# Kernel tuning notes

Hardware: AMD Instinct MI355X
Metric: run time of the kernel (lower is better)

## Reference

```python
import jax, jax.numpy as jnp
import numpy as np

N_STU, N_ITEM, N_CONC = 10000, 50000, 2048
EDGES, K = 250000, 4
EMB, CNUM = 64, 128


def setup_inputs() -> dict:
    key = jax.random.key(0)
    ks = jax.random.split(key, 10)
    return {
        "stu_idx": jax.random.randint(ks[0], (EDGES,), 0, N_STU),
        "item_idx": jax.random.randint(ks[1], (EDGES,), 0, N_ITEM),
        "conc_idx": jax.random.randint(ks[2], (EDGES, K), 0, N_CONC),
        "stu_fusion": jax.random.normal(ks[3], (N_STU, EMB), jnp.float32),
        "item_fusion": jax.random.normal(ks[4], (N_ITEM, EMB), jnp.float32),
        "concept_fusion": jax.random.normal(ks[5], (N_CONC, EMB), jnp.float32),
        # factor weights are non-negative in the original (NoneNegClipper)
        "W_stu": jax.random.uniform(ks[6], (CNUM, 2 * EMB), jnp.float32) * 0.1,
        "W_item": jax.random.uniform(ks[7], (CNUM, 2 * EMB), jnp.float32) * 0.1,
        "w_pred": jax.random.uniform(ks[8], (CNUM,), jnp.float32) * 0.1,
        "b_pred": jax.random.normal(ks[9], (1,), jnp.float32),
    }


def reference(stu_idx, item_idx, conc_idx, stu_fusion, item_fusion,
              concept_fusion, W_stu, W_item, w_pred, b_pred):
    emb = stu_fusion.shape[1]
    # split Linear(2*emb -> CNUM) into the two cat halves: out = x1 @ Wa.T + x2 @ Wb.T
    Ws_a, Ws_b = W_stu[:, :emb], W_stu[:, emb:]
    Wi_a, Wi_b = W_item[:, :emb], W_item[:, emb:]

    # per-entity projections computed once on the tables, then gathered (cheap)
    stu_part = (stu_fusion @ Ws_a.T)[stu_idx]      # [E, CNUM]
    item_part = (item_fusion @ Wi_a.T)[item_idx]   # [E, CNUM]
    conc_stu = (concept_fusion @ Ws_b.T)[conc_idx]   # [E, K, CNUM]
    conc_item = (concept_fusion @ Wi_b.T)[conc_idx]  # [E, K, CNUM]

    stu_out = jax.nn.sigmoid(stu_part[:, None, :] + conc_stu)    # [E, K, CNUM]
    item_out = jax.nn.sigmoid(item_part[:, None, :] + conc_item)  # [E, K, CNUM]
    diff = stu_out - item_out
    per_conc = jax.nn.sigmoid(jnp.einsum('ekc,c->ek', diff, w_pred) + b_pred[0])  # [E, K]
    return per_conc.mean(axis=1)  # [E]
```

## Files before the change

### kernel.cpp

```cpp
#include <hip/hip_runtime.h>
#include <hip/hip_bf16.h>
#include <hip/hip_fp16.h>

constexpr int EDGES = 250000;
constexpr int EMB   = 64;
constexpr int CNUM  = 128;
constexpr int NSTU  = 10000;
constexpr int NITEM = 50000;
constexpr int NCONC = 2048;

constexpr float NEG_LOG2E = -1.44269504088896340736f;

constexpr int STU_JOBS  = NSTU  / 16;
constexpr int ITEM_JOBS = NITEM / 16;
constexpr int CONC_JOBS = (NCONC / 16) * 2;
constexpr int NJOBS     = STU_JOBS + ITEM_JOBS + CONC_JOBS;
constexpr int PROJ_BLKS = (NJOBS + 3) / 4;

typedef _Float16 h8 __attribute__((ext_vector_type(8)));
typedef _Float16 h4 __attribute__((ext_vector_type(4)));
typedef _Float16 h2 __attribute__((ext_vector_type(2)));
typedef float    f32x4 __attribute__((ext_vector_type(4)));
typedef float    f32x2 __attribute__((ext_vector_type(2)));

__device__ __forceinline__ h2 cvt2(float a, float b) {
#if __has_builtin(__builtin_amdgcn_cvt_pkrtz)
    return __builtin_bit_cast(h2, __builtin_amdgcn_cvt_pkrtz(a, b));
#else
    h2 r; r[0] = (_Float16)a; r[1] = (_Float16)b; return r;
#endif
}

__device__ __forceinline__ h8 pack8(float4 lo, float4 hi) {
    const h2 a = cvt2(lo.x, lo.y);
    const h2 b = cvt2(lo.z, lo.w);
    const h2 c = cvt2(hi.x, hi.y);
    const h2 d = cvt2(hi.z, hi.w);
    const h4 ab = __builtin_shufflevector(a, b, 0, 1, 2, 3);
    const h4 cd = __builtin_shufflevector(c, d, 0, 1, 2, 3);
    return __builtin_shufflevector(ab, cd, 0, 1, 2, 3, 4, 5, 6, 7);
}

__device__ __forceinline__ h8 dec8(uint2 v) {
    const f32x2 a = __builtin_amdgcn_cvt_pk_f32_fp8(v.x, false);
    const f32x2 b = __builtin_amdgcn_cvt_pk_f32_fp8(v.x, true);
    const f32x2 c = __builtin_amdgcn_cvt_pk_f32_fp8(v.y, false);
    const f32x2 d = __builtin_amdgcn_cvt_pk_f32_fp8(v.y, true);
    const h2 h0 = cvt2(a[0], a[1]);
    const h2 h1 = cvt2(b[0], b[1]);
    const h2 h2v = cvt2(c[0], c[1]);
    const h2 h3 = cvt2(d[0], d[1]);
    const h4 lo = __builtin_shufflevector(h0, h1, 0, 1, 2, 3);
    const h4 hi = __builtin_shufflevector(h2v, h3, 0, 1, 2, 3);
    return __builtin_shufflevector(lo, hi, 0, 1, 2, 3, 4, 5, 6, 7);
}

template <int CTRL>
__device__ __forceinline__ float dppadd(float x) {
    return x + __int_as_float(__builtin_amdgcn_update_dpp(
        0, __float_as_int(x), CTRL, 0xf, 0xf, true));
}

__global__ __launch_bounds__(256) void proj_mfma(
        const float* __restrict__ stuF, const float* __restrict__ itemF,
        const float* __restrict__ concF,
        const float* __restrict__ W_stu, const float* __restrict__ W_item,
        const float* __restrict__ w_pred,
        unsigned char* __restrict__ ESP8, unsigned char* __restrict__ EIP8,
        _Float16* __restrict__ ECS, _Float16* __restrict__ ECI,
        _Float16* __restrict__ WH) {
    const int tid  = threadIdx.x;
    const int lane = tid & 63;
    const int job  = blockIdx.x * 4 + (tid >> 6);
    if (job >= NJOBS) return;

    if (job == 0) {
        const float2 wv2 = ((const float2*)w_pred)[lane];
        h2 wh; wh[0] = (_Float16)wv2.x; wh[1] = (_Float16)wv2.y;
        *(h2*)(WH + 2 * lane) = wh;
    }

    const float* F; const float* W;
    unsigned char* O8 = nullptr; _Float16* O16 = nullptr;
    int strip, wcol; bool is8;
    if (job < STU_JOBS) {
        F = stuF;  W = W_stu;  O8 = ESP8; strip = job; wcol = 0; is8 = true;
    } else if (job < STU_JOBS + ITEM_JOBS) {
        F = itemF; W = W_item; O8 = EIP8; strip = job - STU_JOBS; wcol = 0;
        is8 = true;
    } else {
        const int g = job - STU_JOBS - ITEM_JOBS;
        F = concF; W = (g & 1) ? W_item : W_stu;
        O16 = (g & 1) ? ECI : ECS;
        strip = g >> 1; wcol = EMB; is8 = false;
    }

    const int m = lane & 15;
    const int q = lane >> 4;
    const int row = strip * 16 + m;

    const float4* fa = (const float4*)(F + (size_t)row * EMB + q * 8);
    const float4* fb = (const float4*)(F + (size_t)row * EMB + 32 + q * 8);
    const h8 A0 = pack8(fa[0], fa[1]);
    const h8 A1 = pack8(fb[0], fb[1]);

    const int orow = strip * 16 + q * 4;

#pragma unroll
    for (int ct = 0; ct < 8; ++ct) {
        const int ch = ct * 16 + m;
        const float* wr = W + (size_t)ch * (2 * EMB) + wcol;
        const float4* wb0 = (const float4*)(wr + q * 8);
        const float4* wb1 = (const float4*)(wr + 32 + q * 8);
        const h8 B0 = pack8(wb0[0], wb0[1]);
        const h8 B1 = pack8(wb1[0], wb1[1]);

        f32x4 acc = {0.f, 0.f, 0.f, 0.f};
        acc = __builtin_amdgcn_mfma_f32_16x16x32_f16(A0, B0, acc, 0, 0, 0);
        acc = __builtin_amdgcn_mfma_f32_16x16x32_f16(A1, B1, acc, 0, 0, 0);

#pragma unroll
        for (int r = 0; r < 4; ++r) {
            const float e = __builtin_amdgcn_exp2f(acc[r] * NEG_LOG2E);
            if (is8) {
                const int pk = __builtin_amdgcn_cvt_pk_fp8_f32(e, e, 0, false);
                O8[(unsigned)(orow + r) * CNUM + ct * 16 + m] =
                    (unsigned char)(pk & 0xff);
            } else {
                O16[(unsigned)(orow + r) * CNUM + ct * 16 + m] = (_Float16)e;
            }
        }
    }
}

__device__ __forceinline__ float sigm(float x) {
    return __builtin_amdgcn_rcpf(1.f + __builtin_amdgcn_exp2f(x * NEG_LOG2E));
}

__global__ __launch_bounds__(256) void edge_kernel(
        const int*  __restrict__ stu_idx,
        const int*  __restrict__ item_idx,
        const int4* __restrict__ conc_idx,
        const unsigned char* __restrict__ ESP8,
        const unsigned char* __restrict__ EIP8,
        const _Float16* __restrict__ ECS,
        const _Float16* __restrict__ ECI,
        const _Float16* __restrict__ WH,
        const float* __restrict__ b_pred,
        float* __restrict__ out) {
    const int lane = threadIdx.x & 63;
    const int wvg  = (blockIdx.x * blockDim.x + threadIdx.x) >> 6;
    const int sub  = lane >> 4;
    const int li   = lane & 15;
    const int e    = wvg * 4 + sub;
    const unsigned co = (unsigned)(li * 8);

    const int s  = stu_idx[e];
    const int it = item_idx[e];
    const int4 c4 = conc_idx[e];

    const uint2 vs8 = *(const uint2*)(ESP8 + (((unsigned)s  << 7) + co));
    const uint2 vi8 = *(const uint2*)(EIP8 + (((unsigned)it << 7) + co));
    const h8 es = dec8(vs8);
    const h8 ei = dec8(vi8);
    const h8 w8 = *(const h8*)(WH + co);
    const float b = b_pred[0];

    const _Float16 O1 = (_Float16)1.f;
    const h8 ONE = {O1, O1, O1, O1, O1, O1, O1, O1};

    const int ck[4] = {c4.x, c4.y, c4.z, c4.w};
    float p[4];
#pragma unroll
    for (int k = 0; k < 4; ++k) {
        const unsigned off = ((unsigned)ck[k] << 7) + co;
        const h8 cs = *(const h8*)(ECS + off);
        const h8 ci = *(const h8*)(ECI + off);
        const h8 Aq = es * cs + ONE;
        const h8 Bq = ei * ci + ONE;
        const h8 dn = Aq * Bq;
        const h8 nm = w8 * (Bq - Aq);
        float N1[4], D1[4];
#pragma unroll
        for (int i = 0; i < 4; ++i) {
            N1[i] = (float)nm[i] * (float)dn[i + 4]
                  + (float)nm[i + 4] * (float)dn[i];
            D1[i] = (float)dn[i] * (float)dn[i + 4];
        }
        const float N2a = N1[0] * D1[2] + N1[2] * D1[0];
        const float N2b = N1[1] * D1[3] + N1[3] * D1[1];
        const float D2a = D1[0] * D1[2];
        const float D2b = D1[1] * D1[3];
        const float N3 = N2a * D2b + N2b * D2a;
        const float D3 = D2a * D2b;
        p[k] = N3 * __builtin_amdgcn_rcpf(D3);
    }

#pragma unroll
    for (int j = 0; j < 4; ++j) p[j] = dppadd<0xB1>(p[j]);
#pragma unroll
    for (int j = 0; j < 4; ++j) p[j] = dppadd<0x4E>(p[j]);
#pragma unroll
    for (int j = 0; j < 4; ++j) p[j] = dppadd<0x141>(p[j]);
#pragma unroll
    for (int j = 0; j < 4; ++j) p[j] = dppadd<0x140>(p[j]);

    const float r = 0.25f * (sigm(p[0] + b) + sigm(p[1] + b) +
                             sigm(p[2] + b) + sigm(p[3] + b));
    if (li == 0) out[e] = r;
}

extern "C" void kernel_launch(void* const* d_in, const int* in_sizes, int n_in,
                              void* d_out, int out_size, void* d_ws, size_t ws_size,
                              hipStream_t stream) {
    const int* stu_idx  = (const int*)d_in[0];
    const int* item_idx = (const int*)d_in[1];
    const int* conc_idx = (const int*)d_in[2];
    const float* stu_fusion     = (const float*)d_in[3];
    const float* item_fusion    = (const float*)d_in[4];
    const float* concept_fusion = (const float*)d_in[5];
    const float* W_stu          = (const float*)d_in[6];
    const float* W_item         = (const float*)d_in[7];
    const float* w_pred         = (const float*)d_in[8];
    const float* b_pred         = (const float*)d_in[9];
    float* out = (float*)d_out;

    unsigned char* ESP8 = (unsigned char*)d_ws;
    unsigned char* EIP8 = ESP8 + (size_t)NSTU * CNUM;
    _Float16* ECS = (_Float16*)(EIP8 + (size_t)NITEM * CNUM);
    _Float16* ECI = ECS + (size_t)NCONC * CNUM;
    _Float16* WH  = ECI + (size_t)NCONC * CNUM;

    proj_mfma<<<PROJ_BLKS, 256, 0, stream>>>(
        stu_fusion, item_fusion, concept_fusion, W_stu, W_item, w_pred,
        ESP8, EIP8, ECS, ECI, WH);

    edge_kernel<<<EDGES / 16, 256, 0, stream>>>(
        stu_idx, item_idx, (const int4*)conc_idx,
        ESP8, EIP8, ECS, ECI, WH, b_pred, out);
}
```

Measured before the change: 136.9 us.

## Store concept projections as interleaved fp8 and fetch both with one load

The concept projection tables for student and item weights change from two separate fp16 arrays to a single fp8 array. Each 8-channel group of the student and item projections is interleaved, so the edge kernel pulls both with one 16-byte load per concept. This halves the bytes per concept gather and removes one load instruction per concept per lane. In exchange it adds fp8 decode work in the inner loop and lowers the precision of the concept factors.

```diff
diff --git a/kernel.cpp b/kernel.cpp
--- a/kernel.cpp
+++ b/kernel.cpp
@@ -41,18 +41,18 @@
     return __builtin_shufflevector(ab, cd, 0, 1, 2, 3, 4, 5, 6, 7);
 }
 
-__device__ __forceinline__ h8 dec8(uint2 v) {
-    const f32x2 a = __builtin_amdgcn_cvt_pk_f32_fp8(v.x, false);
-    const f32x2 b = __builtin_amdgcn_cvt_pk_f32_fp8(v.x, true);
-    const f32x2 c = __builtin_amdgcn_cvt_pk_f32_fp8(v.y, false);
-    const f32x2 d = __builtin_amdgcn_cvt_pk_f32_fp8(v.y, true);
+__device__ __forceinline__ h8 dec8(unsigned lo, unsigned hi) {
+    const f32x2 a = __builtin_amdgcn_cvt_pk_f32_fp8(lo, false);
+    const f32x2 b = __builtin_amdgcn_cvt_pk_f32_fp8(lo, true);
+    const f32x2 c = __builtin_amdgcn_cvt_pk_f32_fp8(hi, false);
+    const f32x2 d = __builtin_amdgcn_cvt_pk_f32_fp8(hi, true);
     const h2 h0 = cvt2(a[0], a[1]);
     const h2 h1 = cvt2(b[0], b[1]);
     const h2 h2v = cvt2(c[0], c[1]);
     const h2 h3 = cvt2(d[0], d[1]);
-    const h4 lo = __builtin_shufflevector(h0, h1, 0, 1, 2, 3);
-    const h4 hi = __builtin_shufflevector(h2v, h3, 0, 1, 2, 3);
-    return __builtin_shufflevector(lo, hi, 0, 1, 2, 3, 4, 5, 6, 7);
+    const h4 lo4 = __builtin_shufflevector(h0, h1, 0, 1, 2, 3);
+    const h4 hi4 = __builtin_shufflevector(h2v, h3, 0, 1, 2, 3);
+    return __builtin_shufflevector(lo4, hi4, 0, 1, 2, 3, 4, 5, 6, 7);
 }
 
 template <int CTRL>
@@ -67,7 +67,7 @@
         const float* __restrict__ W_stu, const float* __restrict__ W_item,
         const float* __restrict__ w_pred,
         unsigned char* __restrict__ ESP8, unsigned char* __restrict__ EIP8,
-        _Float16* __restrict__ ECS, _Float16* __restrict__ ECI,
+        unsigned char* __restrict__ ECB,
         _Float16* __restrict__ WH) {
     const int tid  = threadIdx.x;
     const int lane = tid & 63;
@@ -80,19 +80,18 @@
         *(h2*)(WH + 2 * lane) = wh;
     }
 
-    const float* F; const float* W;
-    unsigned char* O8 = nullptr; _Float16* O16 = nullptr;
-    int strip, wcol; bool is8;
+    const float* F; const float* W; unsigned char* O8;
+    int strip, wcol, sel = 0; bool isconc;
     if (job < STU_JOBS) {
-        F = stuF;  W = W_stu;  O8 = ESP8; strip = job; wcol = 0; is8 = true;
+        F = stuF;  W = W_stu;  O8 = ESP8; strip = job; wcol = 0;
+        isconc = false;
     } else if (job < STU_JOBS + ITEM_JOBS) {
         F = itemF; W = W_item; O8 = EIP8; strip = job - STU_JOBS; wcol = 0;
-        is8 = true;
+        isconc = false;
     } else {
         const int g = job - STU_JOBS - ITEM_JOBS;
-        F = concF; W = (g & 1) ? W_item : W_stu;
-        O16 = (g & 1) ? ECI : ECS;
-        strip = g >> 1; wcol = EMB; is8 = false;
+        F = concF; W = (g & 1) ? W_item : W_stu; O8 = ECB;
+        sel = g & 1; strip = g >> 1; wcol = EMB; isconc = true;
     }
 
     const int m = lane & 15;
@@ -122,13 +121,16 @@
 #pragma unroll
         for (int r = 0; r < 4; ++r) {
             const float e = __builtin_amdgcn_exp2f(acc[r] * NEG_LOG2E);
-            if (is8) {
-                const int pk = __builtin_amdgcn_cvt_pk_fp8_f32(e, e, 0, false);
-                O8[(unsigned)(orow + r) * CNUM + ct * 16 + m] =
-                    (unsigned char)(pk & 0xff);
+            const int pk = __builtin_amdgcn_cvt_pk_fp8_f32(e, e, 0, false);
+            unsigned off;
+            if (!isconc) {
+                off = (unsigned)(orow + r) * CNUM + (unsigned)ch;
             } else {
-                O16[(unsigned)(orow + r) * CNUM + ct * 16 + m] = (_Float16)e;
+                off = (unsigned)(orow + r) * (2 * CNUM)
+                    + (((unsigned)ch >> 3) << 4) + ((unsigned)sel << 3)
+                    + ((unsigned)ch & 7);
             }
+            O8[off] = (unsigned char)(pk & 0xff);
         }
     }
 }
@@ -143,8 +145,7 @@
         const int4* __restrict__ conc_idx,
         const unsigned char* __restrict__ ESP8,
         const unsigned char* __restrict__ EIP8,
-        const _Float16* __restrict__ ECS,
-        const _Float16* __restrict__ ECI,
+        const unsigned char* __restrict__ ECB,
         const _Float16* __restrict__ WH,
         const float* __restrict__ b_pred,
         float* __restrict__ out) {
@@ -161,8 +162,8 @@
 
     const uint2 vs8 = *(const uint2*)(ESP8 + (((unsigned)s  << 7) + co));
     const uint2 vi8 = *(const uint2*)(EIP8 + (((unsigned)it << 7) + co));
-    const h8 es = dec8(vs8);
-    const h8 ei = dec8(vi8);
+    const h8 es = dec8(vs8.x, vs8.y);
+    const h8 ei = dec8(vi8.x, vi8.y);
     const h8 w8 = *(const h8*)(WH + co);
     const float b = b_pred[0];
 
@@ -173,9 +174,10 @@
     float p[4];
 #pragma unroll
     for (int k = 0; k < 4; ++k) {
-        const unsigned off = ((unsigned)ck[k] << 7) + co;
-        const h8 cs = *(const h8*)(ECS + off);
-        const h8 ci = *(const h8*)(ECI + off);
+        const uint4 vv = *(const uint4*)(ECB + (((unsigned)ck[k] << 8)
+                                               + (co << 1)));
+        const h8 cs = dec8(vv.x, vv.y);
+        const h8 ci = dec8(vv.z, vv.w);
         const h8 Aq = es * cs + ONE;
         const h8 Bq = ei * ci + ONE;
         const h8 dn = Aq * Bq;
@@ -227,15 +229,14 @@
 
     unsigned char* ESP8 = (unsigned char*)d_ws;
     unsigned char* EIP8 = ESP8 + (size_t)NSTU * CNUM;
-    _Float16* ECS = (_Float16*)(EIP8 + (size_t)NITEM * CNUM);
-    _Float16* ECI = ECS + (size_t)NCONC * CNUM;
-    _Float16* WH  = ECI + (size_t)NCONC * CNUM;
+    unsigned char* ECB  = EIP8 + (size_t)NITEM * CNUM;
+    _Float16* WH = (_Float16*)(ECB + (size_t)NCONC * 2 * CNUM);
 
     proj_mfma<<<PROJ_BLKS, 256, 0, stream>>>(
         stu_fusion, item_fusion, concept_fusion, W_stu, W_item, w_pred,
-        ESP8, EIP8, ECS, ECI, WH);
+        ESP8, EIP8, ECB, WH);
 
     edge_kernel<<<EDGES / 16, 256, 0, stream>>>(
         stu_idx, item_idx, (const int4*)conc_idx,
-        ESP8, EIP8, ECS, ECI, WH, b_pred, out);
-}
+        ESP8, EIP8, ECB, WH, b_pred, out);
+}
```

Measured after the change: 144.7 us. 1.06x slower.
